# Optimization experiments

Hardware: AMD Instinct MI355X
Metric: run time of the kernel (lower is better)

Reference implementation:

```python
import jax, jax.numpy as jnp
import numpy as np

N_NODES = 100000
N_EDGES = 1600000
IN_DIM = 128
HIDDEN = 128
N_GRAPHS = 64


def setup_inputs() -> dict:
    key = jax.random.key(0)
    ks = jax.random.split(key, 14)
    w = lambda k, shape: jax.random.normal(k, shape, jnp.float32) * 0.05
    return {
        "x": jax.random.normal(ks[0], (N_NODES, IN_DIM), jnp.float32),
        "edge_index": jax.random.randint(ks[1], (2, N_EDGES), 0, N_NODES),
        "batch": jnp.sort(jax.random.randint(ks[2], (N_NODES,), 0, N_GRAPHS)),
        # SAGEConv layer 0: lin_l (on aggregated neighbors, with bias), lin_r (on root, no bias)
        "Wl0": w(ks[3], (IN_DIM, HIDDEN)), "bl0": jnp.zeros((HIDDEN,), jnp.float32), "Wr0": w(ks[4], (IN_DIM, HIDDEN)),
        # SAGEConv layer 1
        "Wl1": w(ks[5], (HIDDEN, HIDDEN)), "bl1": jnp.zeros((HIDDEN,), jnp.float32), "Wr1": w(ks[6], (HIDDEN, HIDDEN)),
        # GlobalAttention gate_nn: Linear(h,h) -> GELU -> Linear(h,1)
        "Wg1": w(ks[7], (HIDDEN, HIDDEN)), "bg1": jnp.zeros((HIDDEN,), jnp.float32),
        "Wg2": w(ks[8], (HIDDEN, 1)), "bg2": jnp.zeros((1,), jnp.float32),
        # head: Linear(h,1)
        "Wh": w(ks[9], (HIDDEN, 1)), "bh": jnp.zeros((1,), jnp.float32),
    }


def _sage_conv(x, src, dst, Wl, bl, Wr):
    # PyG SAGEConv(aggr='mean'): out = lin_l(mean_{j in N(i)} x_j) + lin_r(x_i)
    msg = x[src]                                                   # [E, D] gather
    agg = jax.ops.segment_sum(msg, dst, num_segments=N_NODES)     # [N, D] scatter-add
    cnt = jax.ops.segment_sum(jnp.ones((src.shape[0], 1), x.dtype), dst, num_segments=N_NODES)
    agg = agg / jnp.maximum(cnt, 1.0)                              # mean (0 for isolated nodes)
    return agg @ Wl + bl + x @ Wr


def reference(x, edge_index, batch, Wl0, bl0, Wr0, Wl1, bl1, Wr1, Wg1, bg1, Wg2, bg2, Wh, bh):
    src, dst = edge_index[0], edge_index[1]
    gelu = lambda t: jax.nn.gelu(t, approximate=False)  # torch nn.GELU default (erf)
    h = gelu(_sage_conv(x, src, dst, Wl0, bl0, Wr0))    # dropout is identity at inference
    h = gelu(_sage_conv(h, src, dst, Wl1, bl1, Wr1))
    # GlobalAttention pooling: per-graph softmax over gate scores
    gate = gelu(h @ Wg1 + bg1) @ Wg2 + bg2              # [N, 1]
    gmax = jax.ops.segment_max(gate, batch, num_segments=N_GRAPHS)  # [G, 1]
    e = jnp.exp(gate - gmax[batch])
    denom = jax.ops.segment_sum(e, batch, num_segments=N_GRAPHS)
    alpha = e / denom[batch]                            # [N, 1]
    g = jax.ops.segment_sum(alpha * h, batch, num_segments=N_GRAPHS)  # [G, H]
    return (g @ Wh + bh).reshape(-1)                    # [G] logits
```

## Files before the change

kernel.cpp:

```cpp
#include <hip/hip_runtime.h>
#include <math.h>

#define NN 100000
#define NE 1600000
#define NG 64
#define NBK 1024
#define BKSHIFT 7

typedef unsigned short u16;
typedef unsigned int u32;
typedef __attribute__((ext_vector_type(8))) short short8;
typedef __attribute__((ext_vector_type(4))) float f32x4;

__device__ __forceinline__ float gelu_f(float x) {
    return 0.5f * x * (1.0f + erff(x * 0.7071067811865475f));
}
__device__ __forceinline__ u16 f2bf(float f) {
    u32 u = __float_as_uint(f);
    u32 r = u + 0x7FFFu + ((u >> 16) & 1u);
    return (u16)(r >> 16);
}
__device__ __forceinline__ float bf2f(u16 h) { return __uint_as_float(((u32)h) << 16); }
__device__ __forceinline__ u32 packf(float v) {
    u16 h = f2bf(v);
    u16 l = f2bf(v - bf2f(h));
    return (((u32)h) << 16) | (u32)l;
}
__device__ __forceinline__ float unpackf(u32 p) {
    return __uint_as_float(p & 0xFFFF0000u) + __uint_as_float(p << 16);
}
__device__ __forceinline__ void unpack8(uint4 q0, uint4 q1, short8& hi, short8& lo) {
    u32 v[8] = {q0.x, q0.y, q0.z, q0.w, q1.x, q1.y, q1.z, q1.w};
#pragma unroll
    for (int e = 0; e < 8; ++e) {
        hi[e] = (short)(v[e] >> 16);
        lo[e] = (short)(v[e] & 0xFFFFu);
    }
}
__device__ __forceinline__ void cvt8f(float4 f0, float4 f1, short8& hi, short8& lo) {
    float v[8] = {f0.x, f0.y, f0.z, f0.w, f1.x, f1.y, f1.z, f1.w};
#pragma unroll
    for (int e = 0; e < 8; ++e) {
        u16 h = f2bf(v[e]);
        hi[e] = (short)h;
        lo[e] = (short)f2bf(v[e] - bf2f(h));
    }
}
#define MFMA __builtin_amdgcn_mfma_f32_16x16x32_bf16

__global__ __launch_bounds__(256) void k_bhist(const int* __restrict__ dstp, int* __restrict__ bcnt) {
    __shared__ int h[NBK];
    for (int i = threadIdx.x; i < NBK; i += 256) h[i] = 0;
    __syncthreads();
    int per = (NE + gridDim.x - 1) / gridDim.x;
    int beg = blockIdx.x * per;
    int end = beg + per; if (end > NE) end = NE;
    for (int e = beg + threadIdx.x; e < end; e += 256)
        atomicAdd(&h[dstp[e] >> BKSHIFT], 1);
    __syncthreads();
    for (int i = threadIdx.x; i < NBK; i += 256)
        if (h[i]) atomicAdd(&bcnt[i], h[i]);
}

__global__ __launch_bounds__(NBK) void k_bscan(const int* __restrict__ bcnt, int* __restrict__ boff,
                                               int* __restrict__ bcur) {
    __shared__ int s[NBK];
    int tid = threadIdx.x;
    int v = bcnt[tid];
    int run = v;
    s[tid] = v;
    __syncthreads();
    for (int off = 1; off < NBK; off <<= 1) {
        int t = (tid >= off) ? s[tid - off] : 0;
        __syncthreads();
        run += t;
        s[tid] = run;
        __syncthreads();
    }
    boff[tid] = run - v;
    bcur[tid] = run - v;
}

__global__ __launch_bounds__(256) void k_bscat(const int* __restrict__ srcp, const int* __restrict__ dstp,
                                               int* __restrict__ bcur, int* __restrict__ srcS,
                                               int* __restrict__ dstS) {
    __shared__ int h[NBK];
    __shared__ int basew[NBK];
    for (int i = threadIdx.x; i < NBK; i += 256) h[i] = 0;
    __syncthreads();
    int per = (NE + gridDim.x - 1) / gridDim.x;
    int beg = blockIdx.x * per;
    int end = beg + per; if (end > NE) end = NE;
    for (int e = beg + threadIdx.x; e < end; e += 256)
        atomicAdd(&h[dstp[e] >> BKSHIFT], 1);
    __syncthreads();
    for (int i = threadIdx.x; i < NBK; i += 256) {
        int c = h[i];
        basew[i] = c ? atomicAdd(&bcur[i], c) : 0;
        h[i] = 0;
    }
    __syncthreads();
    for (int e = beg + threadIdx.x; e < end; e += 256) {
        int sv = srcp[e], d = dstp[e];
        int b = d >> BKSHIFT;
        int r = atomicAdd(&h[b], 1);
        int p = basew[b] + r;
        srcS[p] = sv;
        dstS[p] = d;
    }
}

__global__ void k_hist(const int* __restrict__ dstp, int* __restrict__ cnt) {
    int e = blockIdx.x * 256 + threadIdx.x;
    if (e < NE) atomicAdd(&cnt[dstp[e]], 1);
}

#define SB 1024
__global__ __launch_bounds__(SB) void k_scan1(const int* __restrict__ cnt, int* __restrict__ rowp,
                                              int* __restrict__ blksum) {
    __shared__ int s[SB];
    int tid = threadIdx.x;
    int i = blockIdx.x * SB + tid;
    int v = (i < NN) ? cnt[i] : 0;
    int run = v;
    s[tid] = v;
    __syncthreads();
    for (int off = 1; off < SB; off <<= 1) {
        int t = (tid >= off) ? s[tid - off] : 0;
        __syncthreads();
        run += t;
        s[tid] = run;
        __syncthreads();
    }
    if (i < NN) rowp[i] = run - v;
    if (tid == SB - 1) blksum[blockIdx.x] = run;
}

__global__ void k_scan2(const int* __restrict__ blksum, int* __restrict__ blkoff, int nb) {
    __shared__ int s[128];
    int tid = threadIdx.x;
    int v = (tid < nb) ? blksum[tid] : 0;
    int run = v;
    s[tid] = v;
    __syncthreads();
    for (int off = 1; off < 128; off <<= 1) {
        int t = (tid >= off) ? s[tid - off] : 0;
        __syncthreads();
        run += t;
        s[tid] = run;
        __syncthreads();
    }
    if (tid < nb) blkoff[tid] = run - v;
}

__global__ void k_scan3(int* __restrict__ rowp, const int* __restrict__ blkoff,
                        int* __restrict__ rowp2) {
    int i = blockIdx.x * 256 + threadIdx.x;
    if (i < NN) {
        int v = rowp[i] + blkoff[i >> 10];
        rowp[i] = v;
        rowp2[i] = v;
    } else if (i == NN) {
        rowp[NN] = NE;
    }
}

__global__ void k_fscat(const int* __restrict__ srcS, const int* __restrict__ dstS,
                        int* __restrict__ rowp2, int* __restrict__ cidx) {
    int e = blockIdx.x * 256 + threadIdx.x;
    if (e < NE) {
        int pos = atomicAdd(&rowp2[dstS[e]], 1);
        cidx[pos] = srcS[e];
    }
}

__global__ __launch_bounds__(256) void k_repack_bf(const float* __restrict__ x, u16* __restrict__ xbf) {
    int i = blockIdx.x * 256 + threadIdx.x;
    if (i >= NN * 32) return;
    float4 v = ((const float4*)x)[i];
    ushort4 o;
    o.x = f2bf(v.x); o.y = f2bf(v.y); o.z = f2bf(v.z); o.w = f2bf(v.w);
    ((ushort4*)xbf)[i] = o;
}

__global__ __launch_bounds__(256) void k_agg_bf(const u16* __restrict__ xbf, const int* __restrict__ rowp,
                                                const int* __restrict__ cidx, u32* __restrict__ agg) {
    int tid = blockIdx.x * 256 + threadIdx.x;
    int node = tid >> 5;
    int lane = tid & 31;
    if (node >= NN) return;
    int beg = rowp[node], endp = rowp[node + 1];
    const ushort4* x4 = (const ushort4*)xbf;
    float s0 = 0.f, s1 = 0.f, s2 = 0.f, s3 = 0.f;
    int e = beg;
    for (; e + 7 < endp; e += 8) {
        int idx[8];
#pragma unroll
        for (int u = 0; u < 8; ++u) idx[u] = cidx[e + u];
        ushort4 q[8];
#pragma unroll
        for (int u = 0; u < 8; ++u) q[u] = x4[(size_t)idx[u] * 32 + lane];
#pragma unroll
        for (int u = 0; u < 8; ++u) {
            s0 += bf2f(q[u].x); s1 += bf2f(q[u].y);
            s2 += bf2f(q[u].z); s3 += bf2f(q[u].w);
        }
    }
    for (; e < endp; ++e) {
        ushort4 q = x4[(size_t)cidx[e] * 32 + lane];
        s0 += bf2f(q.x); s1 += bf2f(q.y); s2 += bf2f(q.z); s3 += bf2f(q.w);
    }
    float inv = 1.0f / fmaxf((float)(endp - beg), 1.0f);
    uint4 o;
    o.x = packf(s0 * inv); o.y = packf(s1 * inv); o.z = packf(s2 * inv); o.w = packf(s3 * inv);
    ((uint4*)agg)[(size_t)node * 32 + lane] = o;
}

__global__ __launch_bounds__(256) void k_cvtw(const float* __restrict__ W0, const float* __restrict__ W1,
                                              const float* __restrict__ W2, const float* __restrict__ W3,
                                              const float* __restrict__ W4, u16* __restrict__ dst) {
    int idx = blockIdx.x * 256 + threadIdx.x;
    int m = idx >> 14;
    int r = idx & 16383;
    int k = r >> 7, c = r & 127;
    const float* W = (m == 0) ? W0 : (m == 1) ? W1 : (m == 2) ? W2 : (m == 3) ? W3 : W4;
    float v = W[k * 128 + c];
    u16 h = f2bf(v);
    u16 l = f2bf(v - bf2f(h));
    u16* base = dst + (size_t)m * 32768;
    base[c * 128 + k] = h;
    base[16384 + c * 128 + k] = l;
}

template <int A2F32, int WRITEBF>
__global__ __launch_bounds__(512, 2) void k_sage_mf(const u32* A1, const u16* __restrict__ w1hi,
                                                    const u16* __restrict__ w1lo, const float* __restrict__ b1,
                                                    const void* A2v, const u16* __restrict__ w2hi,
                                                    const u16* __restrict__ w2lo, u32* out,
                                                    u16* __restrict__ outbf) {
    __shared__ u16 lds[4][128][40];
    const int t = threadIdx.x;
    const int lane = t & 63;
    const int w = t >> 6;
    const int l15 = lane & 15;
    const int lg = lane >> 4;
    const int n0 = blockIdx.x * 256 + w * 32;
    f32x4 acc[2][8];
#pragma unroll
    for (int ti = 0; ti < 2; ++ti)
#pragma unroll
        for (int ct = 0; ct < 8; ++ct) acc[ti][ct] = (f32x4){0.f, 0.f, 0.f, 0.f};
    int nA = n0 + l15;
    int nB = n0 + 16 + l15;
    if (nA >= NN) nA = NN - 1;
    if (nB >= NN) nB = NN - 1;
    const u32* a1A = A1 + (size_t)nA * 128;
    const u32* a1B = A1 + (size_t)nB * 128;
    const u32* a2Ap = (const u32*)A2v + (size_t)nA * 128;
    const u32* a2Bp = (const u32*)A2v + (size_t)nB * 128;
    const float* a2Af = (const float*)A2v + (size_t)nA * 128;
    const float* a2Bf = (const float*)A2v + (size_t)nB * 128;
    const int koff = 8 * lg;

    uint4 p1A[2][2], p1B[2][2];
    uint4 p2A[2][2], p2B[2][2];
    float4 f2A[2][2], f2B[2][2];

    {
        const uint4* q;
        q = (const uint4*)(a1A + koff); p1A[0][0] = q[0]; p1A[0][1] = q[1];
        q = (const uint4*)(a1B + koff); p1B[0][0] = q[0]; p1B[0][1] = q[1];
        if (A2F32) {
            const float4* f;
            f = (const float4*)(a2Af + koff); f2A[0][0] = f[0]; f2A[0][1] = f[1];
            f = (const float4*)(a2Bf + koff); f2B[0][0] = f[0]; f2B[0][1] = f[1];
        } else {
            const uint4* q2;
            q2 = (const uint4*)(a2Ap + koff); p2A[0][0] = q2[0]; p2A[0][1] = q2[1];
            q2 = (const uint4*)(a2Bp + koff); p2B[0][0] = q2[0]; p2B[0][1] = q2[1];
        }
    }
#pragma unroll
    for (int kb = 0; kb < 4; ++kb) {
        const int k0 = kb * 32;
        const int cur = kb & 1, nxt = cur ^ 1;
        __syncthreads();
        {
            int s = t >> 7, c = t & 127;
            const u16* src = (s == 0) ? w1hi : (s == 1) ? w1lo : (s == 2) ? w2hi : w2lo;
            const uint4* s4 = (const uint4*)(src + (size_t)c * 128 + k0);
            uint4* d4 = (uint4*)&lds[s][c][0];
            d4[0] = s4[0]; d4[1] = s4[1]; d4[2] = s4[2]; d4[3] = s4[3];
        }
        __syncthreads();
        if (kb < 3) {
            const int kn = k0 + 32 + koff;
            const uint4* q;
            q = (const uint4*)(a1A + kn); p1A[nxt][0] = q[0]; p1A[nxt][1] = q[1];
            q = (const uint4*)(a1B + kn); p1B[nxt][0] = q[0]; p1B[nxt][1] = q[1];
            if (A2F32) {
                const float4* f;
                f = (const float4*)(a2Af + kn); f2A[nxt][0] = f[0]; f2A[nxt][1] = f[1];
                f = (const float4*)(a2Bf + kn); f2B[nxt][0] = f[0]; f2B[nxt][1] = f[1];
            } else {
                const uint4* q2;
                q2 = (const uint4*)(a2Ap + kn); p2A[nxt][0] = q2[0]; p2A[nxt][1] = q2[1];
                q2 = (const uint4*)(a2Bp + kn); p2B[nxt][0] = q2[0]; p2B[nxt][1] = q2[1];
            }
        }
        short8 h1A, l1A, h1B, l1B, h2A, l2A, h2B, l2B;
        unpack8(p1A[cur][0], p1A[cur][1], h1A, l1A);
        unpack8(p1B[cur][0], p1B[cur][1], h1B, l1B);
        if (A2F32) {
            cvt8f(f2A[cur][0], f2A[cur][1], h2A, l2A);
            cvt8f(f2B[cur][0], f2B[cur][1], h2B, l2B);
        } else {
            unpack8(p2A[cur][0], p2A[cur][1], h2A, l2A);
            unpack8(p2B[cur][0], p2B[cur][1], h2B, l2B);
        }
#pragma unroll
        for (int ct = 0; ct < 8; ++ct) {
            int c = ct * 16 + l15;
            short8 bh1 = *(const short8*)&lds[0][c][koff];
            short8 bl1 = *(const short8*)&lds[1][c][koff];
            short8 bh2 = *(const short8*)&lds[2][c][koff];
            short8 bl2 = *(const short8*)&lds[3][c][koff];
            acc[0][ct] = MFMA(h1A, bh1, acc[0][ct], 0, 0, 0);
            acc[0][ct] = MFMA(l1A, bh1, acc[0][ct], 0, 0, 0);
            acc[0][ct] = MFMA(h1A, bl1, acc[0][ct], 0, 0, 0);
            acc[0][ct] = MFMA(h2A, bh2, acc[0][ct], 0, 0, 0);
            acc[0][ct] = MFMA(l2A, bh2, acc[0][ct], 0, 0, 0);
            acc[0][ct] = MFMA(h2A, bl2, acc[0][ct], 0, 0, 0);
            acc[1][ct] = MFMA(h1B, bh1, acc[1][ct], 0, 0, 0);
            acc[1][ct] = MFMA(l1B, bh1, acc[1][ct], 0, 0, 0);
            acc[1][ct] = MFMA(h1B, bl1, acc[1][ct], 0, 0, 0);
            acc[1][ct] = MFMA(h2B, bh2, acc[1][ct], 0, 0, 0);
            acc[1][ct] = MFMA(l2B, bh2, acc[1][ct], 0, 0, 0);
            acc[1][ct] = MFMA(h2B, bl2, acc[1][ct], 0, 0, 0);
        }
    }
#pragma unroll
    for (int ti = 0; ti < 2; ++ti) {
#pragma unroll
        for (int ct = 0; ct < 8; ++ct) {
            int c = ct * 16 + l15;
            float bb = b1[c];
#pragma unroll
            for (int r = 0; r < 4; ++r) {
                int node = n0 + ti * 16 + lg * 4 + r;
                if (node < NN) {
                    float v = gelu_f(acc[ti][ct][r] + bb);
                    u32 p = packf(v);
                    out[(size_t)node * 128 + c] = p;
                    if (WRITEBF) outbf[(size_t)node * 128 + c] = (u16)(p >> 16);
                }
            }
        }
    }
}

__global__ __launch_bounds__(512, 2) void k_gatef_mf(const u32* __restrict__ H, const u16* __restrict__ wghi,
                                                     const u16* __restrict__ wglo, const float* __restrict__ bg1,
                                                     const float* __restrict__ Wg2, float* __restrict__ gate) {
    __shared__ u16 lds[2][128][40];
    const int t = threadIdx.x;
    const int lane = t & 63;
    const int w = t >> 6;
    const int l15 = lane & 15;
    const int lg = lane >> 4;
    const int n0 = blockIdx.x * 256 + w * 32;
    f32x4 acc[2][8];
#pragma unroll
    for (int ti = 0; ti < 2; ++ti)
#pragma unroll
        for (int ct = 0; ct < 8; ++ct) acc[ti][ct] = (f32x4){0.f, 0.f, 0.f, 0.f};
    int nA = n0 + l15;
    int nB = n0 + 16 + l15;
    if (nA >= NN) nA = NN - 1;
    if (nB >= NN) nB = NN - 1;
    const u32* hA = H + (size_t)nA * 128;
    const u32* hB = H + (size_t)nB * 128;
    const int koff = 8 * lg;
    uint4 pA[2][2], pB[2][2];
    {
        const uint4* q;
        q = (const uint4*)(hA + koff); pA[0][0] = q[0]; pA[0][1] = q[1];
        q = (const uint4*)(hB + koff); pB[0][0] = q[0]; pB[0][1] = q[1];
    }
#pragma unroll
    for (int kb = 0; kb < 4; ++kb) {
        const int k0 = kb * 32;
        const int cur = kb & 1, nxt = cur ^ 1;
        __syncthreads();
        if (t < 256) {
            int s = t >> 7, c = t & 127;
            const u16* src = (s == 0) ? wghi : wglo;
            const uint4* s4 = (const uint4*)(src + (size_t)c * 128 + k0);
            uint4* d4 = (uint4*)&lds[s][c][0];
            d4[0] = s4[0]; d4[1] = s4[1]; d4[2] = s4[2]; d4[3] = s4[3];
        }
        __syncthreads();
        if (kb < 3) {
            const int kn = k0 + 32 + koff;
            const uint4* q;
            q = (const uint4*)(hA + kn); pA[nxt][0] = q[0]; pA[nxt][1] = q[1];
            q = (const uint4*)(hB + kn); pB[nxt][0] = q[0]; pB[nxt][1] = q[1];
        }
        short8 hAh, hAl, hBh, hBl;
        unpack8(pA[cur][0], pA[cur][1], hAh, hAl);
        unpack8(pB[cur][0], pB[cur][1], hBh, hBl);
#pragma unroll
        for (int ct = 0; ct < 8; ++ct) {
            int c = ct * 16 + l15;
            short8 bh = *(const short8*)&lds[0][c][koff];
            short8 bl = *(const short8*)&lds[1][c][koff];
            acc[0][ct] = MFMA(hAh, bh, acc[0][ct], 0, 0, 0);
            acc[0][ct] = MFMA(hAl, bh, acc[0][ct], 0, 0, 0);
            acc[0][ct] = MFMA(hAh, bl, acc[0][ct], 0, 0, 0);
            acc[1][ct] = MFMA(hBh, bh, acc[1][ct], 0, 0, 0);
            acc[1][ct] = MFMA(hBl, bh, acc[1][ct], 0, 0, 0);
            acc[1][ct] = MFMA(hBh, bl, acc[1][ct], 0, 0, 0);
        }
    }
    float p[2][4];
#pragma unroll
    for (int ti = 0; ti < 2; ++ti)
#pragma unroll
        for (int r = 0; r < 4; ++r) p[ti][r] = 0.f;
#pragma unroll
    for (int ct = 0; ct < 8; ++ct) {
        int c = ct * 16 + l15;
        float bb = bg1[c];
        float gv = Wg2[c];
#pragma unroll
        for (int ti = 0; ti < 2; ++ti)
#pragma unroll
            for (int r = 0; r < 4; ++r) p[ti][r] += gelu_f(acc[ti][ct][r] + bb) * gv;
    }
#pragma unroll
    for (int m = 1; m < 16; m <<= 1) {
#pragma unroll
        for (int ti = 0; ti < 2; ++ti)
#pragma unroll
            for (int r = 0; r < 4; ++r) p[ti][r] += __shfl_xor(p[ti][r], m);
    }
    if (l15 == 0) {
#pragma unroll
        for (int ti = 0; ti < 2; ++ti)
#pragma unroll
            for (int r = 0; r < 4; ++r) {
                int node = n0 + ti * 16 + lg * 4 + r;
                if (node < NN) gate[node] = p[ti][r];
            }
    }
}

__global__ __launch_bounds__(512) void k_pstats(const float* __restrict__ gate, const int* __restrict__ batch,
                                                float* __restrict__ gm, float* __restrict__ gden) {
    int g = blockIdx.x;
    int lo = 0, hi = NN;
    while (lo < hi) { int mid = (lo + hi) >> 1; if (batch[mid] < g) lo = mid + 1; else hi = mid; }
    int start = lo;
    lo = start; hi = NN;
    while (lo < hi) { int mid = (lo + hi) >> 1; if (batch[mid] < g + 1) lo = mid + 1; else hi = mid; }
    int endp = lo;

    __shared__ float red[512];
    int tid = threadIdx.x;

    float m = -1e30f;
    for (int i = start + tid; i < endp; i += 512) m = fmaxf(m, gate[i]);
    red[tid] = m;
    __syncthreads();
    for (int off = 256; off; off >>= 1) {
        if (tid < off) red[tid] = fmaxf(red[tid], red[tid + off]);
        __syncthreads();
    }
    m = red[0];
    __syncthreads();

    float s = 0.f;
    for (int i = start + tid; i < endp; i += 512) s += expf(gate[i] - m);
    red[tid] = s;
    __syncthreads();
    for (int off = 256; off; off >>= 1) {
        if (tid < off) red[tid] += red[tid + off];
        __syncthreads();
    }
    if (tid == 0) { gm[g] = m; gden[g] = red[0]; }
}

__global__ __launch_bounds__(512) void k_pacc(const u32* __restrict__ H, const float* __restrict__ gate,
                                              const int* __restrict__ batch, const float* __restrict__ gm,
                                              const float* __restrict__ gden, float* __restrict__ gacc) {
    int c = threadIdx.x & 127;
    int h = threadIdx.x >> 7;
    int n0 = blockIdx.x * 128;
    int nend = n0 + 128;
    if (nend > NN) nend = NN;
    int i = n0 + h;
    if (i >= nend) return;
    int cur = batch[i];
    float m = gm[cur], invd = 1.0f / gden[cur];
    float acc = 0.f;
    for (; i < nend; i += 4) {
        int gi = batch[i];
        if (gi != cur) {
            atomicAdd(&gacc[cur * 128 + c], acc * invd);
            acc = 0.f;
            cur = gi;
            m = gm[cur];
            invd = 1.0f / gden[cur];
        }
        acc = fmaf(expf(gate[i] - m), unpackf(H[(size_t)i * 128 + c]), acc);
    }
    atomicAdd(&gacc[cur * 128 + c], acc * invd);
}

__global__ __launch_bounds__(64) void k_head(const float* __restrict__ gacc, const float* __restrict__ Wh,
                                             const float* __restrict__ bh, float* __restrict__ out) {
    int g = blockIdx.x;
    int l = threadIdx.x;
    float v = gacc[g * 128 + l] * Wh[l] + gacc[g * 128 + 64 + l] * Wh[64 + l];
#pragma unroll
    for (int m = 1; m < 64; m <<= 1) v += __shfl_xor(v, m);
    if (l == 0) out[g] = v + bh[0];
}

extern "C" void kernel_launch(void* const* d_in, const int* in_sizes, int n_in,
                              void* d_out, int out_size, void* d_ws, size_t ws_size,
                              hipStream_t stream) {
    (void)in_sizes; (void)n_in; (void)out_size; (void)ws_size;
    const float* x   = (const float*)d_in[0];
    const int*  ei   = (const int*)d_in[1];
    const int*  batch= (const int*)d_in[2];
    const float* Wl0 = (const float*)d_in[3];
    const float* bl0 = (const float*)d_in[4];
    const float* Wr0 = (const float*)d_in[5];
    const float* Wl1 = (const float*)d_in[6];
    const float* bl1 = (const float*)d_in[7];
    const float* Wr1 = (const float*)d_in[8];
    const float* Wg1 = (const float*)d_in[9];
    const float* bg1 = (const float*)d_in[10];
    const float* Wg2 = (const float*)d_in[11];
    const float* Wh  = (const float*)d_in[13];
    const float* bh  = (const float*)d_in[14];
    float* out = (float*)d_out;

    const int* srcp = ei;
    const int* dstp = ei + NE;

    char* w = (char*)d_ws;
    size_t off = 0;
    auto alloc = [&](size_t bytes) { void* p = w + off; off += (bytes + 255) & ~(size_t)255; return p; };
    u32* AGG   = (u32*)alloc((size_t)NN * 128 * 4);
    u32* H1    = (u32*)alloc((size_t)NN * 128 * 4);
    u16* XBF   = (u16*)alloc((size_t)NN * 128 * 2);
    u16* H1BF  = (u16*)alloc((size_t)NN * 128 * 2);
    float* gate  = (float*)alloc((size_t)NN * 4);
    int* cnt     = (int*)alloc((size_t)NN * 4);
    int* rowp    = (int*)alloc((size_t)(NN + 1) * 4);
    int* rowp2   = (int*)alloc((size_t)NN * 4);
    int* cidx    = (int*)alloc((size_t)NE * 4);
    int* srcS    = (int*)alloc((size_t)NE * 4);
    int* dstS    = (int*)alloc((size_t)NE * 4);
    int* bcnt    = (int*)alloc(NBK * 4);
    int* boff    = (int*)alloc(NBK * 4);
    int* bcur    = (int*)alloc(NBK * 4);
    int* blksum  = (int*)alloc(128 * 4);
    int* blkoff  = (int*)alloc(128 * 4);
    float* gm    = (float*)alloc(NG * 4);
    float* gden  = (float*)alloc(NG * 4);
    float* gacc  = (float*)alloc((size_t)NG * 128 * 4);
    u16* wt      = (u16*)alloc((size_t)5 * 32768 * 2);

    hipMemsetAsync(cnt, 0, (size_t)NN * 4, stream);
    hipMemsetAsync(bcnt, 0, NBK * 4, stream);
    hipMemsetAsync(gacc, 0, (size_t)NG * 128 * 4, stream);

    k_cvtw<<<320, 256, 0, stream>>>(Wl0, Wr0, Wl1, Wr1, Wg1, wt);
    k_repack_bf<<<(NN * 32 + 255) / 256, 256, 0, stream>>>(x, XBF);

    k_bhist<<<256, 256, 0, stream>>>(dstp, bcnt);
    k_bscan<<<1, NBK, 0, stream>>>(bcnt, boff, bcur);
    k_bscat<<<256, 256, 0, stream>>>(srcp, dstp, bcur, srcS, dstS);
    k_hist<<<(NE + 255) / 256, 256, 0, stream>>>(dstS, cnt);
    int nb = (NN + SB - 1) / SB;
    k_scan1<<<nb, SB, 0, stream>>>(cnt, rowp, blksum);
    k_scan2<<<1, 128, 0, stream>>>(blksum, blkoff, nb);
    k_scan3<<<(NN + 1 + 255) / 256, 256, 0, stream>>>(rowp, blkoff, rowp2);
    k_fscat<<<(NE + 255) / 256, 256, 0, stream>>>(srcS, dstS, rowp2, cidx);

    int gs = (NN + 255) / 256;
    int ga = (NN * 32 + 255) / 256;
    u16* Wl0hi = wt;
    u16* Wl0lo = wt + 16384;
    u16* Wr0hi = wt + 32768;
    u16* Wr0lo = wt + 49152;
    u16* Wl1hi = wt + 65536;
    u16* Wl1lo = wt + 81920;
    u16* Wr1hi = wt + 98304;
    u16* Wr1lo = wt + 114688;
    u16* Wg1hi = wt + 131072;
    u16* Wg1lo = wt + 147456;
    k_agg_bf<<<ga, 256, 0, stream>>>(XBF, rowp, cidx, AGG);
    k_sage_mf<1, 1><<<gs, 512, 0, stream>>>(AGG, Wl0hi, Wl0lo, bl0, x, Wr0hi, Wr0lo, H1, H1BF);
    k_agg_bf<<<ga, 256, 0, stream>>>(H1BF, rowp, cidx, AGG);
    k_sage_mf<0, 0><<<gs, 512, 0, stream>>>(AGG, Wl1hi, Wl1lo, bl1, H1, Wr1hi, Wr1lo, AGG, (u16*)nullptr);
    k_gatef_mf<<<gs, 512, 0, stream>>>(AGG, Wg1hi, Wg1lo, bg1, Wg2, gate);
    k_pstats<<<NG, 512, 0, stream>>>(gate, batch, gm, gden);
    k_pacc<<<(NN + 127) / 128, 512, 0, stream>>>(AGG, gate, batch, gm, gden, gacc);
    k_head<<<NG, 64, 0, stream>>>(gacc, Wh, bh, out);
}
```

Before: 451.0 us.

## Build CSR per destination bucket in shared memory instead of global scans

Edge bucket scatter now writes packed (src,dst) pairs into one array. A new per-bucket kernel counts degrees, prefix-sums them and fills the column indices using shared-memory atomics. This replaces the global degree histogram, the three-kernel scan and the global-atomic fill scatter, cutting several launches and a lot of global atomic and memory traffic. Bucket kernels also move to 512-thread blocks. The cost is that CSR fill order within a row still depends on atomic order, and each block of the new kernel reads its bucket's edges twice.

```diff
diff --git a/kernel.cpp b/kernel.cpp
--- a/kernel.cpp
+++ b/kernel.cpp
@@ -48,17 +48,17 @@
 }
 #define MFMA __builtin_amdgcn_mfma_f32_16x16x32_bf16
 
-__global__ __launch_bounds__(256) void k_bhist(const int* __restrict__ dstp, int* __restrict__ bcnt) {
+__global__ __launch_bounds__(512) void k_bhist(const int* __restrict__ dstp, int* __restrict__ bcnt) {
     __shared__ int h[NBK];
-    for (int i = threadIdx.x; i < NBK; i += 256) h[i] = 0;
+    for (int i = threadIdx.x; i < NBK; i += 512) h[i] = 0;
     __syncthreads();
     int per = (NE + gridDim.x - 1) / gridDim.x;
     int beg = blockIdx.x * per;
     int end = beg + per; if (end > NE) end = NE;
-    for (int e = beg + threadIdx.x; e < end; e += 256)
+    for (int e = beg + threadIdx.x; e < end; e += 512)
         atomicAdd(&h[dstp[e] >> BKSHIFT], 1);
     __syncthreads();
-    for (int i = threadIdx.x; i < NBK; i += 256)
+    for (int i = threadIdx.x; i < NBK; i += 512)
         if (h[i]) atomicAdd(&bcnt[i], h[i]);
 }
 
@@ -81,96 +81,70 @@
     bcur[tid] = run - v;
 }
 
-__global__ __launch_bounds__(256) void k_bscat(const int* __restrict__ srcp, const int* __restrict__ dstp,
-                                               int* __restrict__ bcur, int* __restrict__ srcS,
-                                               int* __restrict__ dstS) {
+__global__ __launch_bounds__(512) void k_bscat(const int* __restrict__ srcp, const int* __restrict__ dstp,
+                                               int* __restrict__ bcur, uint2* __restrict__ esS) {
     __shared__ int h[NBK];
     __shared__ int basew[NBK];
-    for (int i = threadIdx.x; i < NBK; i += 256) h[i] = 0;
+    for (int i = threadIdx.x; i < NBK; i += 512) h[i] = 0;
     __syncthreads();
     int per = (NE + gridDim.x - 1) / gridDim.x;
     int beg = blockIdx.x * per;
     int end = beg + per; if (end > NE) end = NE;
-    for (int e = beg + threadIdx.x; e < end; e += 256)
+    for (int e = beg + threadIdx.x; e < end; e += 512)
         atomicAdd(&h[dstp[e] >> BKSHIFT], 1);
     __syncthreads();
-    for (int i = threadIdx.x; i < NBK; i += 256) {
+    for (int i = threadIdx.x; i < NBK; i += 512) {
         int c = h[i];
         basew[i] = c ? atomicAdd(&bcur[i], c) : 0;
         h[i] = 0;
     }
     __syncthreads();
-    for (int e = beg + threadIdx.x; e < end; e += 256) {
+    for (int e = beg + threadIdx.x; e < end; e += 512) {
         int sv = srcp[e], d = dstp[e];
         int b = d >> BKSHIFT;
         int r = atomicAdd(&h[b], 1);
-        int p = basew[b] + r;
-        srcS[p] = sv;
-        dstS[p] = d;
-    }
-}
-
-__global__ void k_hist(const int* __restrict__ dstp, int* __restrict__ cnt) {
-    int e = blockIdx.x * 256 + threadIdx.x;
-    if (e < NE) atomicAdd(&cnt[dstp[e]], 1);
-}
-
-#define SB 1024
-__global__ __launch_bounds__(SB) void k_scan1(const int* __restrict__ cnt, int* __restrict__ rowp,
-                                              int* __restrict__ blksum) {
-    __shared__ int s[SB];
-    int tid = threadIdx.x;
-    int i = blockIdx.x * SB + tid;
-    int v = (i < NN) ? cnt[i] : 0;
-    int run = v;
-    s[tid] = v;
-    __syncthreads();
-    for (int off = 1; off < SB; off <<= 1) {
-        int t = (tid >= off) ? s[tid - off] : 0;
-        __syncthreads();
-        run += t;
-        s[tid] = run;
-        __syncthreads();
-    }
-    if (i < NN) rowp[i] = run - v;
-    if (tid == SB - 1) blksum[blockIdx.x] = run;
-}
-
-__global__ void k_scan2(const int* __restrict__ blksum, int* __restrict__ blkoff, int nb) {
+        uint2 ed; ed.x = (u32)sv; ed.y = (u32)d;
+        esS[basew[b] + r] = ed;
+    }
+}
+
+__global__ __launch_bounds__(256) void k_csr(const uint2* __restrict__ esS, const int* __restrict__ boff,
+                                             int* __restrict__ rowp, int* __restrict__ cidx) {
+    int b = blockIdx.x;
+    int node0 = b << BKSHIFT;
+    int t = threadIdx.x;
+    __shared__ int cnt0[128];
     __shared__ int s[128];
-    int tid = threadIdx.x;
-    int v = (tid < nb) ? blksum[tid] : 0;
-    int run = v;
-    s[tid] = v;
+    __shared__ int cur[128];
+    if (t < 128) cnt0[t] = 0;
+    __syncthreads();
+    int ebeg = boff[b];
+    int eend = boff[b + 1];
+    for (int e = ebeg + t; e < eend; e += 256)
+        atomicAdd(&cnt0[(int)esS[e].y - node0], 1);
+    __syncthreads();
+    int v0 = (t < 128) ? cnt0[t] : 0;
+    if (t < 128) s[t] = v0;
     __syncthreads();
     for (int off = 1; off < 128; off <<= 1) {
-        int t = (tid >= off) ? s[tid - off] : 0;
-        __syncthreads();
-        run += t;
-        s[tid] = run;
-        __syncthreads();
-    }
-    if (tid < nb) blkoff[tid] = run - v;
-}
-
-__global__ void k_scan3(int* __restrict__ rowp, const int* __restrict__ blkoff,
-                        int* __restrict__ rowp2) {
-    int i = blockIdx.x * 256 + threadIdx.x;
-    if (i < NN) {
-        int v = rowp[i] + blkoff[i >> 10];
-        rowp[i] = v;
-        rowp2[i] = v;
-    } else if (i == NN) {
-        rowp[NN] = NE;
-    }
-}
-
-__global__ void k_fscat(const int* __restrict__ srcS, const int* __restrict__ dstS,
-                        int* __restrict__ rowp2, int* __restrict__ cidx) {
-    int e = blockIdx.x * 256 + threadIdx.x;
-    if (e < NE) {
-        int pos = atomicAdd(&rowp2[dstS[e]], 1);
-        cidx[pos] = srcS[e];
+        int tmp = (t < 128 && t >= off) ? s[t - off] : 0;
+        __syncthreads();
+        if (t < 128) s[t] += tmp;
+        __syncthreads();
+    }
+    if (t < 128) {
+        int excl = s[t] - v0;
+        cur[t] = excl;
+        int node = node0 + t;
+        if (node < NN) rowp[node] = ebeg + excl;
+    }
+    if (b == gridDim.x - 1 && t == 0) rowp[NN] = NE;
+    __syncthreads();
+    for (int e = ebeg + t; e < eend; e += 256) {
+        uint2 ed = esS[e];
+        int ln = (int)ed.y - node0;
+        int pos = ebeg + atomicAdd(&cur[ln], 1);
+        cidx[pos] = (int)ed.x;
     }
 }
 
@@ -558,38 +532,27 @@
     u16* XBF   = (u16*)alloc((size_t)NN * 128 * 2);
     u16* H1BF  = (u16*)alloc((size_t)NN * 128 * 2);
     float* gate  = (float*)alloc((size_t)NN * 4);
-    int* cnt     = (int*)alloc((size_t)NN * 4);
     int* rowp    = (int*)alloc((size_t)(NN + 1) * 4);
-    int* rowp2   = (int*)alloc((size_t)NN * 4);
     int* cidx    = (int*)alloc((size_t)NE * 4);
-    int* srcS    = (int*)alloc((size_t)NE * 4);
-    int* dstS    = (int*)alloc((size_t)NE * 4);
+    uint2* esS   = (uint2*)alloc((size_t)NE * 8);
     int* bcnt    = (int*)alloc(NBK * 4);
     int* boff    = (int*)alloc(NBK * 4);
     int* bcur    = (int*)alloc(NBK * 4);
-    int* blksum  = (int*)alloc(128 * 4);
-    int* blkoff  = (int*)alloc(128 * 4);
     float* gm    = (float*)alloc(NG * 4);
     float* gden  = (float*)alloc(NG * 4);
     float* gacc  = (float*)alloc((size_t)NG * 128 * 4);
     u16* wt      = (u16*)alloc((size_t)5 * 32768 * 2);
 
-    hipMemsetAsync(cnt, 0, (size_t)NN * 4, stream);
     hipMemsetAsync(bcnt, 0, NBK * 4, stream);
     hipMemsetAsync(gacc, 0, (size_t)NG * 128 * 4, stream);
 
     k_cvtw<<<320, 256, 0, stream>>>(Wl0, Wr0, Wl1, Wr1, Wg1, wt);
     k_repack_bf<<<(NN * 32 + 255) / 256, 256, 0, stream>>>(x, XBF);
 
-    k_bhist<<<256, 256, 0, stream>>>(dstp, bcnt);
+    k_bhist<<<256, 512, 0, stream>>>(dstp, bcnt);
     k_bscan<<<1, NBK, 0, stream>>>(bcnt, boff, bcur);
-    k_bscat<<<256, 256, 0, stream>>>(srcp, dstp, bcur, srcS, dstS);
-    k_hist<<<(NE + 255) / 256, 256, 0, stream>>>(dstS, cnt);
-    int nb = (NN + SB - 1) / SB;
-    k_scan1<<<nb, SB, 0, stream>>>(cnt, rowp, blksum);
-    k_scan2<<<1, 128, 0, stream>>>(blksum, blkoff, nb);
-    k_scan3<<<(NN + 1 + 255) / 256, 256, 0, stream>>>(rowp, blkoff, rowp2);
-    k_fscat<<<(NE + 255) / 256, 256, 0, stream>>>(srcS, dstS, rowp2, cidx);
+    k_bscat<<<256, 512, 0, stream>>>(srcp, dstp, bcur, esS);
+    k_csr<<<(NN + 127) / 128, 256, 0, stream>>>(esS, boff, rowp, cidx);
 
     int gs = (NN + 255) / 256;
     int ga = (NN * 32 + 255) / 256;
```

New measurement: 363.9 us (median of 2 runs). 19.3% less time.
